# Performance work log

Measured on AMD Instinct MI355X. Metric: run time of the kernel, lower is better.

Reference implementation:

```python
import jax, jax.numpy as jnp
import numpy as np

T = 2048
HID = 4096
H = 32
HKV = 8
D = 128
EPS = 1e-5
THETA = 1e6
WINDOW = 1024


def setup_inputs() -> dict:
    key = jax.random.key(0)
    k1, k2, k3 = jax.random.split(key, 3)
    return {
        "positions": jnp.arange(T, dtype=jnp.int32),
        "hidden_states": jax.random.normal(k1, (T, HID), dtype=jnp.float32),
        "w_qkv": jax.random.normal(k2, (HID, (H + 2 * HKV) * D), dtype=jnp.float32) * 0.02,
        "q_norm_w": jnp.ones((D,), dtype=jnp.float32),
        "k_norm_w": jnp.ones((D,), dtype=jnp.float32),
        "w_o": jax.random.normal(k3, (H * D, HID), dtype=jnp.float32) * 0.02,
    }


def _rmsnorm(x, w):
    # per-head RMSNorm over last dim (head_dim)
    var = jnp.mean(x * x, axis=-1, keepdims=True)
    return x * jax.lax.rsqrt(var + EPS) * w


def _rope_neox(x, positions):
    # x: [T, heads, D]; neox style: rotate halves
    half = D // 2
    inv_freq = 1.0 / (THETA ** (jnp.arange(0, half, dtype=jnp.float32) / half))
    ang = positions.astype(jnp.float32)[:, None] * inv_freq  # [T, half]
    cos = jnp.cos(ang)[:, None, :]
    sin = jnp.sin(ang)[:, None, :]
    x1, x2 = x[..., :half], x[..., half:]
    return jnp.concatenate([x1 * cos - x2 * sin, x2 * cos + x1 * sin], axis=-1)


def reference(positions, hidden_states, w_qkv, q_norm_w, k_norm_w, w_o):
    qkv = hidden_states @ w_qkv  # [T, (H+2Hkv)*D]
    q, k, v = jnp.split(qkv, [H * D, (H + HKV) * D], axis=-1)
    q = _rmsnorm(q.reshape(T, H, D), q_norm_w)
    k = _rmsnorm(k.reshape(T, HKV, D), k_norm_w)
    v = v.reshape(T, HKV, D)

    q = _rope_neox(q, positions)
    k = _rope_neox(k, positions)

    # GQA: expand kv heads to H
    rep = H // HKV
    k = jnp.repeat(k, rep, axis=1)  # [T, H, D]
    v = jnp.repeat(v, rep, axis=1)

    scale = D ** -0.5
    scores = jnp.einsum('thd,shd->hts', q, k) * scale  # [H, T, T]
    i = jnp.arange(T)[:, None]
    j = jnp.arange(T)[None, :]
    mask = (j <= i) & (i - j < WINDOW)  # causal + sliding window
    scores = jnp.where(mask[None], scores, -jnp.inf)
    probs = jax.nn.softmax(scores, axis=-1)
    attn = jnp.einsum('hts,shd->thd', probs, v).reshape(T, H * D)
    return attn @ w_o
```

## Files before the change

### kernel.cpp

```cpp
#include <hip/hip_runtime.h>
#include <hip/hip_bf16.h>
#include <stdint.h>

#define T_SEQ  2048
#define HIDDEN 4096
#define NHEAD  32
#define NKV    8
#define HDIM   128
#define NQKV   6144
#define WINDOW 1024
#define SCALE  0.08838834764831845f
#define SHIFT  12.0f

typedef __attribute__((ext_vector_type(8))) short          short8;
typedef __attribute__((ext_vector_type(8))) unsigned short ushort8_t;
typedef __attribute__((ext_vector_type(4))) float          floatx4;

__device__ __forceinline__ unsigned short f2bf(float f) {
    union { float f; unsigned int u; } v; v.f = f;
    unsigned int u = v.u;
    unsigned int r = (u + 0x7FFFu + ((u >> 16) & 1u)) >> 16;
    return (unsigned short)r;
}
__device__ __forceinline__ float bf2f(unsigned short u) {
    union { unsigned int u; float f; } v; v.u = ((unsigned int)u) << 16;
    return v.f;
}

#define GLOBAL_AS(p) ((const __attribute__((address_space(1))) void*)(p))
#define LDS_AS(p)    ((__attribute__((address_space(3))) void*)(p))

__global__ __launch_bounds__(256) void convert_bf16_kernel(
        const float* __restrict__ X, unsigned short* __restrict__ Y, int n4) {
    int i = blockIdx.x * blockDim.x + threadIdx.x;
    if (i < n4) {
        float4 v = ((const float4*)X)[i];
        ushort4 o;
        o.x = f2bf(v.x); o.y = f2bf(v.y); o.z = f2bf(v.z); o.w = f2bf(v.w);
        ((ushort4*)Y)[i] = o;
    }
}

__global__ __launch_bounds__(256) void transpose_bf16_kernel(
        const float* __restrict__ W, unsigned short* __restrict__ Wt, int K, int N) {
    __shared__ float tile[128][33];
    const int n0 = blockIdx.x * 32, k0 = blockIdx.y * 128;
    const int tid = threadIdx.x;
    const int rr = tid >> 3, cc = tid & 7;
    #pragma unroll
    for (int p = 0; p < 4; ++p) {
        int r = p * 32 + rr;
        float4 v = *(const float4*)&W[(size_t)(k0 + r) * N + n0 + cc * 4];
        tile[r][cc * 4 + 0] = v.x; tile[r][cc * 4 + 1] = v.y;
        tile[r][cc * 4 + 2] = v.z; tile[r][cc * 4 + 3] = v.w;
    }
    __syncthreads();
    const int nL = tid >> 3, kc = tid & 7;
    #pragma unroll
    for (int q = 0; q < 2; ++q) {
        int kbase = kc * 8 + q * 64;
        ushort8_t o;
        #pragma unroll
        for (int j = 0; j < 8; ++j) o[j] = f2bf(tile[kbase + j][nL]);
        *(ushort8_t*)&Wt[(size_t)(n0 + nL) * K + k0 + kbase] = o;
    }
}

template <bool BF16_OUT>
__global__ __launch_bounds__(256) void gemm_bt_kernel(
        const unsigned short* __restrict__ A,
        const unsigned short* __restrict__ B,
        void* __restrict__ Cv, int M, int N, int K) {
    __shared__ __align__(16) unsigned short As[128 * 32];
    __shared__ __align__(16) unsigned short Bs[128 * 32];
    const int tid  = threadIdx.x;
    const int lane = tid & 63, wave = tid >> 6;
    const int wr = wave >> 1, wc = wave & 1;
    const int m0 = blockIdx.y * 128, n0 = blockIdx.x * 128;

    floatx4 acc[4][4] = {};
    const int lrow = lane & 15;
    const int lk   = (lane >> 4) * 8;

    for (int k0 = 0; k0 < K; k0 += 32) {
        #pragma unroll
        for (int i = 0; i < 2; ++i) {
            int c = i * 256 + tid;
            const unsigned short* gpA = A + (size_t)(m0 + (c >> 2)) * K + k0 + (c & 3) * 8;
            __builtin_amdgcn_global_load_lds(GLOBAL_AS(gpA), LDS_AS(As + c * 8), 16, 0, 0);
            const unsigned short* gpB = B + (size_t)(n0 + (c >> 2)) * K + k0 + (c & 3) * 8;
            __builtin_amdgcn_global_load_lds(GLOBAL_AS(gpB), LDS_AS(Bs + c * 8), 16, 0, 0);
        }
        __syncthreads();

        short8 af[4], bf[4];
        #pragma unroll
        for (int t = 0; t < 4; ++t) {
            af[t] = *(const short8*)(As + (wr * 64 + t * 16 + lrow) * 32 + lk);
            bf[t] = *(const short8*)(Bs + (wc * 64 + t * 16 + lrow) * 32 + lk);
        }
        #pragma unroll
        for (int ti = 0; ti < 4; ++ti)
            #pragma unroll
            for (int tj = 0; tj < 4; ++tj)
                acc[ti][tj] = __builtin_amdgcn_mfma_f32_16x16x32_bf16(
                    af[ti], bf[tj], acc[ti][tj], 0, 0, 0);
        __syncthreads();
    }

    const int rowb = (lane >> 4) * 4, col = lane & 15;
    #pragma unroll
    for (int ti = 0; ti < 4; ++ti)
        #pragma unroll
        for (int tj = 0; tj < 4; ++tj) {
            size_t base = (size_t)(m0 + wr * 64 + ti * 16 + rowb) * N
                        + (n0 + wc * 64 + tj * 16 + col);
            #pragma unroll
            for (int r = 0; r < 4; ++r) {
                if (BF16_OUT)
                    ((unsigned short*)Cv)[base + (size_t)r * N] = f2bf(acc[ti][tj][r]);
                else
                    ((float*)Cv)[base + (size_t)r * N] = acc[ti][tj][r];
            }
        }
}

__global__ __launch_bounds__(256) void rope_table_kernel(
        const int* __restrict__ positions, float2* __restrict__ rope) {
    int idx = blockIdx.x * 256 + threadIdx.x;
    int t = idx >> 6, i = idx & 63;
    float inv_freq = expf((float)i * -0.2158673524681918f);
    float sn, cs;
    sincosf((float)positions[t] * inv_freq, &sn, &cs);
    rope[idx] = make_float2(cs, sn);
}

__global__ __launch_bounds__(256) void qkv_post_kernel(
        const unsigned short* __restrict__ qkv, const float2* __restrict__ rope,
        const float* __restrict__ qw, const float* __restrict__ kw,
        unsigned short* __restrict__ qb,
        unsigned short* __restrict__ kb,
        unsigned short* __restrict__ vbT) {
    const int head = blockIdx.y;
    const int t0   = blockIdx.x * 32;
    const int tid  = threadIdx.x;

    if (head < 40) {
        const int r  = tid >> 3;
        const int q8 = tid & 7;
        const int t  = t0 + r;
        const unsigned short* src = qkv + (size_t)t * NQKV
                         + (head < 32 ? head * 128 : 4096 + (head - 32) * 128)
                         + q8 * 16;
        const float* w = (head < 32) ? qw : kw;

        ushort8_t u0 = *(const ushort8_t*)src;
        ushort8_t u1 = *(const ushort8_t*)(src + 8);
        float x[16];
        #pragma unroll
        for (int j = 0; j < 8; ++j) { x[j] = bf2f(u0[j]); x[8 + j] = bf2f(u1[j]); }

        float ss = 0.f;
        #pragma unroll
        for (int j = 0; j < 16; ++j) ss = fmaf(x[j], x[j], ss);
        ss += __shfl_xor(ss, 1); ss += __shfl_xor(ss, 2); ss += __shfl_xor(ss, 4);
        float sc = rsqrtf(ss * (1.f / 128.f) + 1e-5f);

        float xn[16], xp[16];
        #pragma unroll
        for (int j = 0; j < 16; ++j) xn[j] = x[j] * sc * w[q8 * 16 + j];
        #pragma unroll
        for (int j = 0; j < 16; ++j) xp[j] = __shfl_xor(xn[j], 4);

        const float2* rp = rope + (size_t)t * 64 + (q8 & 3) * 16;
        ushort8_t o0, o1;
        #pragma unroll
        for (int j = 0; j < 8; ++j) {
            float2 cs = rp[j];
            float res = (q8 < 4) ? (xn[j] * cs.x - xp[j] * cs.y)
                                 : (xn[j] * cs.x + xp[j] * cs.y);
            o0[j] = f2bf(res);
        }
        #pragma unroll
        for (int j = 0; j < 8; ++j) {
            float2 cs = rp[8 + j];
            float res = (q8 < 4) ? (xn[8+j] * cs.x - xp[8+j] * cs.y)
                                 : (xn[8+j] * cs.x + xp[8+j] * cs.y);
            o1[j] = f2bf(res);
        }
        unsigned short* dst = (head < 32)
            ? qb + ((size_t)t * 32 + head) * 128 + q8 * 16
            : kb + ((size_t)t * 8 + (head - 32)) * 128 + q8 * 16;
        *(ushort8_t*)dst       = o0;
        *(ushort8_t*)(dst + 8) = o1;
    } else {
        __shared__ float tile[128][33];
        const int hk = head - 40;
        {
            const int r = tid >> 3, c8 = tid & 7;
            const unsigned short* src =
                qkv + (size_t)(t0 + r) * NQKV + 5120 + hk * 128 + c8 * 16;
            ushort8_t u0 = *(const ushort8_t*)src;
            ushort8_t u1 = *(const ushort8_t*)(src + 8);
            #pragma unroll
            for (int j = 0; j < 8; ++j) {
                tile[c8 * 16 + j][r]     = bf2f(u0[j]);
                tile[c8 * 16 + 8 + j][r] = bf2f(u1[j]);
            }
        }
        __syncthreads();
        {
            const int d = tid >> 1, th = tid & 1;
            ushort8_t o0, o1;
            #pragma unroll
            for (int j = 0; j < 8; ++j) o0[j] = f2bf(tile[d][th * 16 + j]);
            #pragma unroll
            for (int j = 0; j < 8; ++j) o1[j] = f2bf(tile[d][th * 16 + 8 + j]);
            unsigned short* dst = vbT + ((size_t)hk * 128 + d) * T_SEQ + t0 + th * 16;
            *(ushort8_t*)dst       = o0;
            *(ushort8_t*)(dst + 8) = o1;
        }
    }
}

__global__ __launch_bounds__(256) void attention_kernel(
        const unsigned short* __restrict__ qb,
        const unsigned short* __restrict__ kb,
        const unsigned short* __restrict__ vbT,
        unsigned short* __restrict__ attnb) {
    const int h    = blockIdx.x & 31;
    const int Q0   = (blockIdx.x >> 5) * 64;
    const int tid  = threadIdx.x, wave = tid >> 6, lane = tid & 63;
    const int keyA = lane & 15, g = lane >> 4;
    const int hk   = h >> 2;
    const int qlo  = Q0 + wave * 16;

    __shared__ __align__(16) unsigned short ks [32 * 128];
    __shared__ __align__(16) unsigned short vsT[128 * 32];
    __shared__ __align__(16) unsigned short Pa [4 * 16 * 40];

    unsigned short* pw = Pa + wave * 640;

    short8 qa[4];
    {
        const unsigned short* qp = qb + ((size_t)(qlo + keyA) * 32 + h) * 128 + g * 8;
        #pragma unroll
        for (int s = 0; s < 4; ++s) qa[s] = *(const short8*)(qp + s * 32);
    }

    floatx4 acc[8] = {};
    float l_part[4] = {0.f, 0.f, 0.f, 0.f};

    const int s_begin = (Q0 >= WINDOW) ? ((Q0 - (WINDOW - 1)) & ~31) : 0;
    const int s_end   = Q0 + 63;

    for (int s0 = s_begin; s0 <= s_end; s0 += 32) {
        #pragma unroll
        for (int i = 0; i < 2; ++i) {
            int c = i * 256 + tid;
            {   int row = c >> 4, u = c & 15, su = u ^ (row & 7);
                const unsigned short* kp = kb + ((size_t)(s0 + row) * 8 + hk) * 128 + su * 8;
                __builtin_amdgcn_global_load_lds(GLOBAL_AS(kp), LDS_AS(ks + c * 8), 16, 0, 0); }
            {   int d = c >> 2, u = c & 3, su = u ^ (d & 3);
                const unsigned short* vp = vbT + ((size_t)hk * 128 + d) * T_SEQ + s0 + su * 8;
                __builtin_amdgcn_global_load_lds(GLOBAL_AS(vp), LDS_AS(vsT + c * 8), 16, 0, 0); }
        }
        __syncthreads();

        if (s0 <= qlo + 15 && s0 + 31 >= qlo - (WINDOW - 1)) {
            floatx4 sa0 = {}, sa1 = {};
            #pragma unroll
            for (int kst = 0; kst < 4; ++kst) {
                int u = g + 4 * kst;
                short8 k0 = *(const short8*)(ks + keyA * 128 + (u ^ (keyA & 7)) * 8);
                short8 k1 = *(const short8*)(ks + (16 + keyA) * 128 + (u ^ ((16 + keyA) & 7)) * 8);
                sa0 = __builtin_amdgcn_mfma_f32_16x16x32_bf16(qa[kst], k0, sa0, 0, 0, 0);
                sa1 = __builtin_amdgcn_mfma_f32_16x16x32_bf16(qa[kst], k1, sa1, 0, 0, 0);
            }
            float p0[4], p1[4];
            #pragma unroll
            for (int r = 0; r < 4; ++r) {
                int row = qlo + 4 * g + r;
                int sA = s0 + keyA, sB = sA + 16;
                bool vA = (sA <= row) && (row - sA < WINDOW);
                bool vB = (sB <= row) && (row - sB < WINDOW);
                p0[r] = vA ? __expf(fmaf(sa0[r], SCALE, -SHIFT)) : 0.f;
                p1[r] = vB ? __expf(fmaf(sa1[r], SCALE, -SHIFT)) : 0.f;
                l_part[r] += p0[r] + p1[r];
            }
            #pragma unroll
            for (int r = 0; r < 4; ++r) {
                pw[(4 * g + r) * 40 + keyA]      = f2bf(p0[r]);
                pw[(4 * g + r) * 40 + keyA + 16] = f2bf(p1[r]);
            }
            short8 pf = *(const short8*)(pw + keyA * 40 + g * 8);

            #pragma unroll
            for (int t = 0; t < 8; ++t) {
                int d = t * 16 + keyA;
                short8 vf = *(const short8*)(vsT + d * 32 + (g ^ (d & 3)) * 8);
                acc[t] = __builtin_amdgcn_mfma_f32_16x16x32_bf16(pf, vf, acc[t], 0, 0, 0);
            }
        }
        __syncthreads();
    }

    float inv[4];
    #pragma unroll
    for (int r = 0; r < 4; ++r) {
        float l = l_part[r];
        l += __shfl_xor(l, 1); l += __shfl_xor(l, 2);
        l += __shfl_xor(l, 4); l += __shfl_xor(l, 8);
        inv[r] = 1.f / l;
    }
    #pragma unroll
    for (int t = 0; t < 8; ++t)
        #pragma unroll
        for (int r = 0; r < 4; ++r)
            attnb[(size_t)(qlo + 4 * g + r) * 4096 + h * 128 + t * 16 + keyA] =
                f2bf(acc[t][r] * inv[r]);
}

extern "C" void kernel_launch(void* const* d_in, const int* in_sizes, int n_in,
                              void* d_out, int out_size, void* d_ws, size_t ws_size,
                              hipStream_t stream) {
    const int*   positions = (const int*)  d_in[0];
    const float* hs        = (const float*)d_in[1];
    const float* w_qkv     = (const float*)d_in[2];
    const float* q_norm_w  = (const float*)d_in[3];
    const float* k_norm_w  = (const float*)d_in[4];
    const float* w_o       = (const float*)d_in[5];
    float* out = (float*)d_out;

    char* ws = (char*)d_ws;
    unsigned short* hsb   = (unsigned short*)(ws);
    unsigned short* wqkvt = (unsigned short*)(ws + (size_t)(16u << 20));
    unsigned short* wot   = (unsigned short*)(ws + (size_t)(64u << 20));
    unsigned short* qkvb  = (unsigned short*)(ws + (size_t)(96u << 20));
    unsigned short* qb    = (unsigned short*)(ws + (size_t)(16u << 20));
    unsigned short* kb    = (unsigned short*)(ws + (size_t)(32u << 20));
    unsigned short* vbT   = (unsigned short*)(ws + (size_t)(36u << 20));
    float2*         rope  = (float2*)        (ws + (size_t)(40u << 20));
    unsigned short* attnb = hsb;

    convert_bf16_kernel<<<dim3((T_SEQ * HIDDEN / 4 + 255) / 256), 256, 0, stream>>>(
        hs, hsb, T_SEQ * HIDDEN / 4);
    transpose_bf16_kernel<<<dim3(NQKV / 32, HIDDEN / 128), 256, 0, stream>>>(
        w_qkv, wqkvt, HIDDEN, NQKV);
    transpose_bf16_kernel<<<dim3(HIDDEN / 32, HIDDEN / 128), 256, 0, stream>>>(
        w_o, wot, HIDDEN, HIDDEN);
    gemm_bt_kernel<true><<<dim3(NQKV / 128, T_SEQ / 128), 256, 0, stream>>>(
        hsb, wqkvt, qkvb, T_SEQ, NQKV, HIDDEN);
    rope_table_kernel<<<dim3(T_SEQ * 64 / 256), 256, 0, stream>>>(positions, rope);
    qkv_post_kernel<<<dim3(T_SEQ / 32, 48), 256, 0, stream>>>(
        qkvb, rope, q_norm_w, k_norm_w, qb, kb, vbT);
    attention_kernel<<<dim3((T_SEQ / 64) * NHEAD), 256, 0, stream>>>(
        qb, kb, vbT, attnb);
    gemm_bt_kernel<false><<<dim3(HIDDEN / 128, T_SEQ / 128), 256, 0, stream>>>(
        attnb, wot, out, T_SEQ, HIDDEN, HIDDEN);
}
```

Before: 566.7 us.

## Rewrite bf16 GEMM with triple-buffered LDS pipeline, swizzle, and larger tiles

```diff
diff --git a/kernel.cpp b/kernel.cpp
--- a/kernel.cpp
+++ b/kernel.cpp
@@ -30,6 +30,10 @@
 #define GLOBAL_AS(p) ((const __attribute__((address_space(1))) void*)(p))
 #define LDS_AS(p)    ((__attribute__((address_space(3))) void*)(p))
 
+#define S_BARRIER() do { asm volatile("" ::: "memory");  \
+                         __builtin_amdgcn_s_barrier();   \
+                         asm volatile("" ::: "memory"); } while (0)
+
 __global__ __launch_bounds__(256) void convert_bf16_kernel(
         const float* __restrict__ X, unsigned short* __restrict__ Y, int n4) {
     int i = blockIdx.x * blockDim.x + threadIdx.x;
@@ -66,61 +70,122 @@
     }
 }
 
+#define STAGE_A(bufi, t2, r)                                                      \
+    __builtin_amdgcn_global_load_lds(                                             \
+        GLOBAL_AS(A + (size_t)(m0 + rRow[r]) * K + ((t2) << 6) + rOff[r]),        \
+        LDS_AS(&As[bufi][((r) * 512 + tid) * 8]), 16, 0, 0)
+#define STAGE_B(bufi, t2, r)                                                      \
+    __builtin_amdgcn_global_load_lds(                                             \
+        GLOBAL_AS(B + (size_t)(n0 + rRow[r]) * K + ((t2) << 6) + rOff[r]),        \
+        LDS_AS(&Bs[bufi][((r) * 512 + tid) * 8]), 16, 0, 0)
+
+#define KTILE(curb, stgb, t2, DO_STG, VMWAIT) do {                                \
+    const unsigned short* ap = &As[curb][0];                                      \
+    const unsigned short* bp = &Bs[curb][0];                                      \
+    short8 bfr[4][2], afr[2][2];                                                  \
+    _Pragma("unroll") for (int n = 0; n < 4; ++n)                                 \
+        _Pragma("unroll") for (int kh = 0; kh < 2; ++kh)                          \
+            bfr[n][kh] = *(const short8*)(bp + bBase + n * 1024 + (sA0 ^ (kh << 5))); \
+    _Pragma("unroll") for (int m = 0; m < 2; ++m)                                 \
+        _Pragma("unroll") for (int kh = 0; kh < 2; ++kh)                          \
+            afr[m][kh] = *(const short8*)(ap + aBase + m * 1024 + (sA0 ^ (kh << 5))); \
+    if (DO_STG) { STAGE_A(stgb, t2, 0); STAGE_A(stgb, t2, 1); STAGE_B(stgb, t2, 0); } \
+    S_BARRIER();                                                                  \
+    __builtin_amdgcn_s_setprio(1);                                                \
+    _Pragma("unroll") for (int m = 0; m < 2; ++m)                                 \
+        _Pragma("unroll") for (int n = 0; n < 4; ++n) {                           \
+            acc[m][n] = __builtin_amdgcn_mfma_f32_16x16x32_bf16(                  \
+                afr[m][0], bfr[n][0], acc[m][n], 0, 0, 0);                        \
+            acc[m][n] = __builtin_amdgcn_mfma_f32_16x16x32_bf16(                  \
+                afr[m][1], bfr[n][1], acc[m][n], 0, 0, 0);                        \
+        }                                                                         \
+    __builtin_amdgcn_s_setprio(0);                                                \
+    S_BARRIER();                                                                  \
+    _Pragma("unroll") for (int m = 0; m < 2; ++m)                                 \
+        _Pragma("unroll") for (int kh = 0; kh < 2; ++kh)                          \
+            afr[m][kh] = *(const short8*)(ap + aBase + (m + 2) * 1024 + (sA0 ^ (kh << 5))); \
+    if (DO_STG) { STAGE_A(stgb, t2, 2); STAGE_A(stgb, t2, 3); STAGE_B(stgb, t2, 1); } \
+    VMWAIT;                                                                       \
+    S_BARRIER();                                                                  \
+    __builtin_amdgcn_s_setprio(1);                                                \
+    _Pragma("unroll") for (int m = 0; m < 2; ++m)                                 \
+        _Pragma("unroll") for (int n = 0; n < 4; ++n) {                           \
+            acc[m + 2][n] = __builtin_amdgcn_mfma_f32_16x16x32_bf16(              \
+                afr[m][0], bfr[n][0], acc[m + 2][n], 0, 0, 0);                    \
+            acc[m + 2][n] = __builtin_amdgcn_mfma_f32_16x16x32_bf16(              \
+                afr[m][1], bfr[n][1], acc[m + 2][n], 0, 0, 0);                    \
+        }                                                                         \
+    __builtin_amdgcn_s_setprio(0);                                                \
+    S_BARRIER();                                                                  \
+} while (0)
+
 template <bool BF16_OUT>
-__global__ __launch_bounds__(256) void gemm_bt_kernel(
+__global__ __launch_bounds__(512, 2) void gemm_bt2_kernel(
         const unsigned short* __restrict__ A,
         const unsigned short* __restrict__ B,
         void* __restrict__ Cv, int M, int N, int K) {
-    __shared__ __align__(16) unsigned short As[128 * 32];
-    __shared__ __align__(16) unsigned short Bs[128 * 32];
+    __shared__ __align__(16) unsigned short As[3][256 * 64];
+    __shared__ __align__(16) unsigned short Bs[3][128 * 64];
+
     const int tid  = threadIdx.x;
     const int lane = tid & 63, wave = tid >> 6;
     const int wr = wave >> 1, wc = wave & 1;
-    const int m0 = blockIdx.y * 128, n0 = blockIdx.x * 128;
+    const int lrow = lane & 15, hi = lane >> 4;
+
+    const int nwg = gridDim.x * gridDim.y;
+    int wg = blockIdx.y * gridDim.x + blockIdx.x;
+    wg = (wg & 7) * (nwg >> 3) + (wg >> 3);
+    const int bx = wg % gridDim.x;
+    const int by = wg / gridDim.x;
+    const int m0 = by * 256, n0 = bx * 128;
+
+    const int NT = K >> 6;
+
+    int rRow[4], rOff[4];
+    #pragma unroll
+    for (int r = 0; r < 4; ++r) {
+        int idx = r * 512 + tid;
+        int row = idx >> 3;
+        rRow[r] = row;
+        rOff[r] = ((idx & 7) ^ (row & 7)) * 8;
+    }
+
+    const int sA0   = (hi ^ (lrow & 7)) * 8;
+    const int aBase = (wr * 64 + lrow) * 64;
+    const int bBase = (wc * 64 + lrow) * 64;
 
     floatx4 acc[4][4] = {};
-    const int lrow = lane & 15;
-    const int lk   = (lane >> 4) * 8;
-
-    for (int k0 = 0; k0 < K; k0 += 32) {
-        #pragma unroll
-        for (int i = 0; i < 2; ++i) {
-            int c = i * 256 + tid;
-            const unsigned short* gpA = A + (size_t)(m0 + (c >> 2)) * K + k0 + (c & 3) * 8;
-            __builtin_amdgcn_global_load_lds(GLOBAL_AS(gpA), LDS_AS(As + c * 8), 16, 0, 0);
-            const unsigned short* gpB = B + (size_t)(n0 + (c >> 2)) * K + k0 + (c & 3) * 8;
-            __builtin_amdgcn_global_load_lds(GLOBAL_AS(gpB), LDS_AS(Bs + c * 8), 16, 0, 0);
-        }
-        __syncthreads();
-
-        short8 af[4], bf[4];
-        #pragma unroll
-        for (int t = 0; t < 4; ++t) {
-            af[t] = *(const short8*)(As + (wr * 64 + t * 16 + lrow) * 32 + lk);
-            bf[t] = *(const short8*)(Bs + (wc * 64 + t * 16 + lrow) * 32 + lk);
-        }
-        #pragma unroll
-        for (int ti = 0; ti < 4; ++ti)
-            #pragma unroll
-            for (int tj = 0; tj < 4; ++tj)
-                acc[ti][tj] = __builtin_amdgcn_mfma_f32_16x16x32_bf16(
-                    af[ti], bf[tj], acc[ti][tj], 0, 0, 0);
-        __syncthreads();
-    }
-
-    const int rowb = (lane >> 4) * 4, col = lane & 15;
-    #pragma unroll
-    for (int ti = 0; ti < 4; ++ti)
-        #pragma unroll
-        for (int tj = 0; tj < 4; ++tj) {
-            size_t base = (size_t)(m0 + wr * 64 + ti * 16 + rowb) * N
-                        + (n0 + wc * 64 + tj * 16 + col);
+
+    STAGE_A(0, 0, 0); STAGE_A(0, 0, 1); STAGE_A(0, 0, 2); STAGE_A(0, 0, 3);
+    STAGE_B(0, 0, 0); STAGE_B(0, 0, 1);
+    STAGE_A(1, 1, 0); STAGE_A(1, 1, 1); STAGE_A(1, 1, 2); STAGE_A(1, 1, 3);
+    STAGE_B(1, 1, 0); STAGE_B(1, 1, 1);
+    asm volatile("s_waitcnt vmcnt(6)" ::: "memory");
+    S_BARRIER();
+
+    int cur = 0, stg = 2;
+    for (int t = 0; t < NT - 2; ++t) {
+        KTILE(cur, stg, t + 2, true, asm volatile("s_waitcnt vmcnt(6)" ::: "memory"));
+        cur = (cur == 2) ? 0 : cur + 1;
+        stg = (stg == 2) ? 0 : stg + 1;
+    }
+    KTILE(cur, stg, 0, false, asm volatile("s_waitcnt vmcnt(0)" ::: "memory"));
+    cur = (cur == 2) ? 0 : cur + 1;
+    KTILE(cur, stg, 0, false, (void)0);
+
+    const int rowb = hi * 4, col = lrow;
+    #pragma unroll
+    for (int mi = 0; mi < 4; ++mi)
+        #pragma unroll
+        for (int ni = 0; ni < 4; ++ni) {
+            size_t base = (size_t)(m0 + wr * 64 + mi * 16 + rowb) * N
+                        + (n0 + wc * 64 + ni * 16 + col);
             #pragma unroll
             for (int r = 0; r < 4; ++r) {
                 if (BF16_OUT)
-                    ((unsigned short*)Cv)[base + (size_t)r * N] = f2bf(acc[ti][tj][r]);
+                    ((unsigned short*)Cv)[base + (size_t)r * N] = f2bf(acc[mi][ni][r]);
                 else
-                    ((float*)Cv)[base + (size_t)r * N] = acc[ti][tj][r];
+                    ((float*)Cv)[base + (size_t)r * N] = acc[mi][ni][r];
             }
         }
 }
@@ -349,13 +414,13 @@
         w_qkv, wqkvt, HIDDEN, NQKV);
     transpose_bf16_kernel<<<dim3(HIDDEN / 32, HIDDEN / 128), 256, 0, stream>>>(
         w_o, wot, HIDDEN, HIDDEN);
-    gemm_bt_kernel<true><<<dim3(NQKV / 128, T_SEQ / 128), 256, 0, stream>>>(
+    gemm_bt2_kernel<true><<<dim3(NQKV / 128, T_SEQ / 256), 512, 0, stream>>>(
         hsb, wqkvt, qkvb, T_SEQ, NQKV, HIDDEN);
     rope_table_kernel<<<dim3(T_SEQ * 64 / 256), 256, 0, stream>>>(positions, rope);
     qkv_post_kernel<<<dim3(T_SEQ / 32, 48), 256, 0, stream>>>(
         qkvb, rope, q_norm_w, k_norm_w, qb, kb, vbT);
     attention_kernel<<<dim3((T_SEQ / 64) * NHEAD), 256, 0, stream>>>(
         qb, kb, vbT, attnb);
-    gemm_bt_kernel<false><<<dim3(HIDDEN / 128, T_SEQ / 128), 256, 0, stream>>>(
+    gemm_bt2_kernel<false><<<dim3(HIDDEN / 128, T_SEQ / 256), 512, 0, stream>>>(
         attnb, wot, out, T_SEQ, HIDDEN, HIDDEN);
 }
```

Result: faster. 548.7 us (-3.2%).

## Double-buffer GEMM K-tiles with swizzled LDS and XCD-aware block remap

Applied to the files above, without the earlier changes.

```diff
diff --git a/kernel.cpp b/kernel.cpp
--- a/kernel.cpp
+++ b/kernel.cpp
@@ -30,6 +30,10 @@
 #define GLOBAL_AS(p) ((const __attribute__((address_space(1))) void*)(p))
 #define LDS_AS(p)    ((__attribute__((address_space(3))) void*)(p))
 
+#define S_BARRIER() do { asm volatile("" ::: "memory");  \
+                         __builtin_amdgcn_s_barrier();   \
+                         asm volatile("" ::: "memory"); } while (0)
+
 __global__ __launch_bounds__(256) void convert_bf16_kernel(
         const float* __restrict__ X, unsigned short* __restrict__ Y, int n4) {
     int i = blockIdx.x * blockDim.x + threadIdx.x;
@@ -66,61 +70,111 @@
     }
 }
 
+#define STG3_A(bufi, kt, r)                                                       \
+    __builtin_amdgcn_global_load_lds(                                             \
+        GLOBAL_AS(A + (size_t)(m0 + rRow[r]) * K + ((kt) << 6) + rOff[r]),        \
+        LDS_AS(&As3[bufi][((r) * 256 + tid) * 8]), 16, 0, 0)
+#define STG3_B(bufi, kt, r)                                                       \
+    __builtin_amdgcn_global_load_lds(                                             \
+        GLOBAL_AS(B + (size_t)(n0 + rRow[r]) * K + ((kt) << 6) + rOff[r]),        \
+        LDS_AS(&Bs3[bufi][((r) * 256 + tid) * 8]), 16, 0, 0)
+
 template <bool BF16_OUT>
-__global__ __launch_bounds__(256) void gemm_bt_kernel(
+__global__ __launch_bounds__(256, 2) void gemm_bt3_kernel(
         const unsigned short* __restrict__ A,
         const unsigned short* __restrict__ B,
         void* __restrict__ Cv, int M, int N, int K) {
-    __shared__ __align__(16) unsigned short As[128 * 32];
-    __shared__ __align__(16) unsigned short Bs[128 * 32];
+    __shared__ __align__(16) unsigned short As3[2][128 * 64];
+    __shared__ __align__(16) unsigned short Bs3[2][128 * 64];
+
     const int tid  = threadIdx.x;
     const int lane = tid & 63, wave = tid >> 6;
     const int wr = wave >> 1, wc = wave & 1;
-    const int m0 = blockIdx.y * 128, n0 = blockIdx.x * 128;
+    const int lrow = lane & 15, hi = lane >> 4;
+
+    const int nwg = gridDim.x * gridDim.y;
+    int wg = blockIdx.y * gridDim.x + blockIdx.x;
+    wg = (wg & 7) * (nwg >> 3) + (wg >> 3);
+    const int bx = wg % gridDim.x;
+    const int by = wg / gridDim.x;
+    const int m0 = by * 128, n0 = bx * 128;
+
+    const int NT = K >> 6;
+
+    int rRow[4], rOff[4];
+    #pragma unroll
+    for (int r = 0; r < 4; ++r) {
+        int idx = r * 256 + tid;
+        int row = idx >> 3;
+        rRow[r] = row;
+        rOff[r] = ((idx & 7) ^ (row & 7)) * 8;
+    }
+
+    const int sA0   = (hi ^ (lrow & 7)) * 8;
+    const int aBase = (wr * 64 + lrow) * 64;
+    const int bBase = (wc * 64 + lrow) * 64;
 
     floatx4 acc[4][4] = {};
-    const int lrow = lane & 15;
-    const int lk   = (lane >> 4) * 8;
-
-    for (int k0 = 0; k0 < K; k0 += 32) {
-        #pragma unroll
-        for (int i = 0; i < 2; ++i) {
-            int c = i * 256 + tid;
-            const unsigned short* gpA = A + (size_t)(m0 + (c >> 2)) * K + k0 + (c & 3) * 8;
-            __builtin_amdgcn_global_load_lds(GLOBAL_AS(gpA), LDS_AS(As + c * 8), 16, 0, 0);
-            const unsigned short* gpB = B + (size_t)(n0 + (c >> 2)) * K + k0 + (c & 3) * 8;
-            __builtin_amdgcn_global_load_lds(GLOBAL_AS(gpB), LDS_AS(Bs + c * 8), 16, 0, 0);
-        }
-        __syncthreads();
-
-        short8 af[4], bf[4];
-        #pragma unroll
-        for (int t = 0; t < 4; ++t) {
-            af[t] = *(const short8*)(As + (wr * 64 + t * 16 + lrow) * 32 + lk);
-            bf[t] = *(const short8*)(Bs + (wc * 64 + t * 16 + lrow) * 32 + lk);
-        }
-        #pragma unroll
-        for (int ti = 0; ti < 4; ++ti)
-            #pragma unroll
-            for (int tj = 0; tj < 4; ++tj)
-                acc[ti][tj] = __builtin_amdgcn_mfma_f32_16x16x32_bf16(
-                    af[ti], bf[tj], acc[ti][tj], 0, 0, 0);
-        __syncthreads();
-    }
-
-    const int rowb = (lane >> 4) * 4, col = lane & 15;
-    #pragma unroll
-    for (int ti = 0; ti < 4; ++ti)
-        #pragma unroll
-        for (int tj = 0; tj < 4; ++tj) {
-            size_t base = (size_t)(m0 + wr * 64 + ti * 16 + rowb) * N
-                        + (n0 + wc * 64 + tj * 16 + col);
+
+    auto compute_tile = [&](int cur) {
+        const unsigned short* ap = &As3[cur][0];
+        const unsigned short* bp = &Bs3[cur][0];
+        short8 af[4][2], bf[4][2];
+        #pragma unroll
+        for (int m = 0; m < 4; ++m)
+            #pragma unroll
+            for (int kh = 0; kh < 2; ++kh)
+                af[m][kh] = *(const short8*)(ap + aBase + m * 1024 + (sA0 ^ (kh << 5)));
+        #pragma unroll
+        for (int n = 0; n < 4; ++n)
+            #pragma unroll
+            for (int kh = 0; kh < 2; ++kh)
+                bf[n][kh] = *(const short8*)(bp + bBase + n * 1024 + (sA0 ^ (kh << 5)));
+        __builtin_amdgcn_s_setprio(1);
+        #pragma unroll
+        for (int m = 0; m < 4; ++m)
+            #pragma unroll
+            for (int n = 0; n < 4; ++n) {
+                acc[m][n] = __builtin_amdgcn_mfma_f32_16x16x32_bf16(
+                    af[m][0], bf[n][0], acc[m][n], 0, 0, 0);
+                acc[m][n] = __builtin_amdgcn_mfma_f32_16x16x32_bf16(
+                    af[m][1], bf[n][1], acc[m][n], 0, 0, 0);
+            }
+        __builtin_amdgcn_s_setprio(0);
+    };
+
+    #pragma unroll
+    for (int r = 0; r < 4; ++r) STG3_A(0, 0, r);
+    #pragma unroll
+    for (int r = 0; r < 4; ++r) STG3_B(0, 0, r);
+    asm volatile("s_waitcnt vmcnt(0)" ::: "memory");
+    S_BARRIER();
+
+    for (int t = 0; t < NT - 1; ++t) {
+        const int cur = t & 1;
+        #pragma unroll
+        for (int r = 0; r < 4; ++r) STG3_A(cur ^ 1, t + 1, r);
+        #pragma unroll
+        for (int r = 0; r < 4; ++r) STG3_B(cur ^ 1, t + 1, r);
+        compute_tile(cur);
+        asm volatile("s_waitcnt vmcnt(0)" ::: "memory");
+        S_BARRIER();
+    }
+    compute_tile((NT - 1) & 1);
+
+    const int rowb = hi * 4, col = lrow;
+    #pragma unroll
+    for (int mi = 0; mi < 4; ++mi)
+        #pragma unroll
+        for (int ni = 0; ni < 4; ++ni) {
+            size_t base = (size_t)(m0 + wr * 64 + mi * 16 + rowb) * N
+                        + (n0 + wc * 64 + ni * 16 + col);
             #pragma unroll
             for (int r = 0; r < 4; ++r) {
                 if (BF16_OUT)
-                    ((unsigned short*)Cv)[base + (size_t)r * N] = f2bf(acc[ti][tj][r]);
+                    ((unsigned short*)Cv)[base + (size_t)r * N] = f2bf(acc[mi][ni][r]);
                 else
-                    ((float*)Cv)[base + (size_t)r * N] = acc[ti][tj][r];
+                    ((float*)Cv)[base + (size_t)r * N] = acc[mi][ni][r];
             }
         }
 }
@@ -349,13 +403,13 @@
         w_qkv, wqkvt, HIDDEN, NQKV);
     transpose_bf16_kernel<<<dim3(HIDDEN / 32, HIDDEN / 128), 256, 0, stream>>>(
         w_o, wot, HIDDEN, HIDDEN);
-    gemm_bt_kernel<true><<<dim3(NQKV / 128, T_SEQ / 128), 256, 0, stream>>>(
+    gemm_bt3_kernel<true><<<dim3(NQKV / 128, T_SEQ / 128), 256, 0, stream>>>(
         hsb, wqkvt, qkvb, T_SEQ, NQKV, HIDDEN);
     rope_table_kernel<<<dim3(T_SEQ * 64 / 256), 256, 0, stream>>>(positions, rope);
     qkv_post_kernel<<<dim3(T_SEQ / 32, 48), 256, 0, stream>>>(
         qkvb, rope, q_norm_w, k_norm_w, qb, kb, vbT);
     attention_kernel<<<dim3((T_SEQ / 64) * NHEAD), 256, 0, stream>>>(
         qb, kb, vbT, attnb);
-    gemm_bt_kernel<false><<<dim3(HIDDEN / 128, T_SEQ / 128), 256, 0, stream>>>(
+    gemm_bt3_kernel<false><<<dim3(HIDDEN / 128, T_SEQ / 128), 256, 0, stream>>>(
         attnb, wot, out, T_SEQ, HIDDEN, HIDDEN);
 }
```

Result: faster. 552.6 us (-2.5%).
